# Optimization experiments

Hardware: AMD Instinct MI355X
Metric: run time of the kernel (lower is better)

The kernel has to match this reference:

```python
import jax, jax.numpy as jnp
import numpy as np

TEMPERATURE = 8.0  # sqrt(d_k=64)

def setup_inputs() -> dict:
    key = jax.random.key(0)
    kq, kk, kv, km1, km2 = jax.random.split(key, 5)
    B, Lq, Lk, D = 128, 512, 512, 64
    q = jax.random.normal(kq, (B, Lq, D), dtype=jnp.float32)
    k = jax.random.normal(kk, (B, Lk, D), dtype=jnp.float32)
    v = jax.random.normal(kv, (B, Lk, D), dtype=jnp.float32)
    key_mask = jax.random.bernoulli(km1, 0.5, (B, Lq, Lk))
    query_mask = jax.random.bernoulli(km2, 0.5, (B, Lq, Lk))
    return {"q": q, "k": k, "v": v, "key_mask": key_mask, "query_mask": query_mask}

def reference(q, k, v, key_mask, query_mask):
    # attn = (q @ k^T) / temperature, pre-softmax key masking with -inf
    scores = jnp.einsum('bqd,bkd->bqk', q, k) / TEMPERATURE
    scores = jnp.where(key_mask, -jnp.inf, scores)
    attn = jax.nn.softmax(scores, axis=-1)
    # post-softmax query-row zeroing
    attn = jnp.where(query_mask, 0.0, attn)
    # dropout omitted (eval mode / deterministic reference)
    output = jnp.einsum('bqk,bkd->bqd', attn, v)
    return (output, attn)
```

## Files before the change

kernel.cpp:

```cpp
#include <hip/hip_runtime.h>
#include <hip/hip_bf16.h>

#define BATCH 128
#define LQ    512
#define LK    512
#define DH    64
#define TQ    16
#define KC    64

#define VROW  72
#define SSTR  520

typedef float    float4v __attribute__((ext_vector_type(4)));
typedef short    short8v __attribute__((ext_vector_type(8)));
typedef short    short4v __attribute__((ext_vector_type(4)));
typedef int      int4v   __attribute__((ext_vector_type(4)));
typedef _Float16 half4v  __attribute__((ext_vector_type(4)));

__device__ __forceinline__ short bf16r(float f) {
  union { float f; unsigned u; } x; x.f = f;
  unsigned r = x.u + 0x7FFFu + ((x.u >> 16) & 1u);
  return (short)(r >> 16);
}

__global__ __launch_bounds__(256, 6)
void sdpa_kernel(const float* __restrict__ Q, const float* __restrict__ K,
                 const float* __restrict__ V, const int* __restrict__ KM,
                 const int* __restrict__ QM, float* __restrict__ OUT,
                 float* __restrict__ ATT)
{
  __shared__ short kvs[KC * VROW];
  __shared__ short scs[TQ * SSTR];

  const int bid  = blockIdx.x;
  const int wg   = ((bid & 7) << 9) | (bid >> 3);
  const int b    = wg >> 5;
  const int q0   = (wg & 31) * TQ;
  const int tid  = threadIdx.x;
  const int lane = tid & 63;
  const int wave = tid >> 6;
  const int lm   = lane & 15;
  const int quad = lane >> 4;

  const int row = tid >> 4;
  const int col = tid & 15;
  const size_t gro = (size_t)(b * LQ + q0 + row) * LK;

  int4v kmv[8];
#pragma unroll
  for (int j = 0; j < 8; ++j)
    kmv[j] = __builtin_nontemporal_load((const int4v*)(KM + gro + col * 4 + j * 64));

  const float* qrow = Q + ((size_t)(b * LQ + q0 + lm)) * DH + quad * 8;
  short8v aq0, aq1;
  {
    float4v f0 = *(const float4v*)(qrow + 0);
    float4v f1 = *(const float4v*)(qrow + 4);
    float4v f2 = *(const float4v*)(qrow + 32);
    float4v f3 = *(const float4v*)(qrow + 36);
#pragma unroll
    for (int e = 0; e < 4; ++e) {
      aq0[e]     = bf16r(f0[e]);
      aq0[e + 4] = bf16r(f1[e]);
      aq1[e]     = bf16r(f2[e]);
      aq1[e + 4] = bf16r(f3[e]);
    }
  }

#pragma unroll
  for (int t = 0; t < 8; ++t) {
    const int T = wave * 8 + t;
    const float* kr = K + ((size_t)(b * LK + T * 16 + lm)) * DH + quad * 8;
    float4v f0 = *(const float4v*)(kr + 0);
    float4v f1 = *(const float4v*)(kr + 4);
    float4v f2 = *(const float4v*)(kr + 32);
    float4v f3 = *(const float4v*)(kr + 36);
    short8v b0, b1;
#pragma unroll
    for (int e = 0; e < 4; ++e) {
      b0[e]     = bf16r(f0[e]);
      b0[e + 4] = bf16r(f1[e]);
      b1[e]     = bf16r(f2[e]);
      b1[e + 4] = bf16r(f3[e]);
    }
    float4v acc = {0.f, 0.f, 0.f, 0.f};
    acc = __builtin_amdgcn_mfma_f32_16x16x32_bf16(aq0, b0, acc, 0, 0, 0);
    acc = __builtin_amdgcn_mfma_f32_16x16x32_bf16(aq1, b1, acc, 0, 0, 0);
    const int n  = T * 16 + lm;
    const int m0 = quad * 4;
#pragma unroll
    for (int j = 0; j < 4; ++j)
      *(_Float16*)&scs[(m0 + j) * SSTR + n] = (_Float16)acc[j];
  }
  __syncthreads();

  float s[32];
  float mx = -INFINITY;
#pragma unroll
  for (int j = 0; j < 8; ++j) {
    half4v h4 = *(const half4v*)&scs[row * SSTR + col * 4 + j * 64];
#pragma unroll
    for (int e = 0; e < 4; ++e) {
      float val = kmv[j][e] ? -INFINITY : (float)h4[e];
      s[j * 4 + e] = val;
      mx = fmaxf(mx, val);
    }
  }
  int4v qmv[8];
#pragma unroll
  for (int j = 0; j < 8; ++j)
    qmv[j] = __builtin_nontemporal_load((const int4v*)(QM + gro + col * 4 + j * 64));
#pragma unroll
  for (int off = 8; off; off >>= 1) mx = fmaxf(mx, __shfl_xor(mx, off, 64));
  float sum = 0.f;
#pragma unroll
  for (int j = 0; j < 32; ++j) {
    float p = __expf((s[j] - mx) * 0.125f);
    s[j] = p;
    sum += p;
  }
#pragma unroll
  for (int off = 8; off; off >>= 1) sum += __shfl_xor(sum, off, 64);
  const float inv = 1.f / sum;
  float* arow = ATT + gro;
#pragma unroll
  for (int j = 0; j < 8; ++j) {
    int kk = col * 4 + j * 64;
    float4v a4;
#pragma unroll
    for (int e = 0; e < 4; ++e)
      a4[e] = qmv[j][e] ? 0.f : s[j * 4 + e] * inv;
    __builtin_nontemporal_store(a4, (float4v*)(arow + kk));
    short4v ab;
    ab[0] = bf16r(a4[0]); ab[1] = bf16r(a4[1]);
    ab[2] = bf16r(a4[2]); ab[3] = bf16r(a4[3]);
    *(short4v*)&scs[row * SSTR + kk] = ab;
  }

  float4v oacc = {0.f, 0.f, 0.f, 0.f};
  const float* vbase = V + ((size_t)b * LK) * DH;
  float4v va[4];
  {
    const float* vp = vbase + (row * 4) * DH + col * 4;
#pragma unroll
    for (int r = 0; r < 4; ++r) va[r] = *(const float4v*)(vp + r * DH);
  }
#pragma unroll
  for (int kt = 0; kt < 8; ++kt) {
#pragma unroll
    for (int e = 0; e < 4; ++e) {
      int d  = col * 4 + e;
      int gp = row ^ (d & 15);
      short4v s4;
      s4[0] = bf16r(va[0][e]); s4[1] = bf16r(va[1][e]);
      s4[2] = bf16r(va[2][e]); s4[3] = bf16r(va[3][e]);
      *(short4v*)&kvs[d * VROW + gp * 4] = s4;
    }
    float4v vb[4];
    if (kt < 7) {
      const float* vp = vbase + ((kt + 1) * KC + row * 4) * DH + col * 4;
#pragma unroll
      for (int r = 0; r < 4; ++r) vb[r] = *(const float4v*)(vp + r * DH);
    }
    __syncthreads();
#pragma unroll
    for (int ks = 0; ks < 2; ++ks) {
      const short* ap = &scs[lm * SSTR + kt * KC + ks * 32 + quad * 8];
      short8v a8 = *(const short8v*)ap;
      int n  = wave * 16 + lm;
      int g0 = ks * 8 + quad * 2;
      short4v lo = *(const short4v*)&kvs[n * VROW + ((g0    ) ^ (n & 15)) * 4];
      short4v hi = *(const short4v*)&kvs[n * VROW + ((g0 + 1) ^ (n & 15)) * 4];
      short8v b8;
      b8[0] = lo[0]; b8[1] = lo[1]; b8[2] = lo[2]; b8[3] = lo[3];
      b8[4] = hi[0]; b8[5] = hi[1]; b8[6] = hi[2]; b8[7] = hi[3];
      oacc = __builtin_amdgcn_mfma_f32_16x16x32_bf16(a8, b8, oacc, 0, 0, 0);
    }
    __syncthreads();
#pragma unroll
    for (int r = 0; r < 4; ++r) va[r] = vb[r];
  }
  {
    int m0 = quad * 4;
    float* obase = OUT + ((size_t)(b * LQ + q0 + m0)) * DH + wave * 16 + lm;
    obase[0 * DH] = oacc[0];
    obase[1 * DH] = oacc[1];
    obase[2 * DH] = oacc[2];
    obase[3 * DH] = oacc[3];
  }
}

extern "C" void kernel_launch(void* const* d_in, const int* in_sizes, int n_in,
                              void* d_out, int out_size, void* d_ws, size_t ws_size,
                              hipStream_t stream) {
  const float* q  = (const float*)d_in[0];
  const float* k  = (const float*)d_in[1];
  const float* v  = (const float*)d_in[2];
  const int*   km = (const int*)d_in[3];
  const int*   qm = (const int*)d_in[4];
  float* out  = (float*)d_out;
  float* attn = out + (size_t)BATCH * LQ * DH;
  dim3 grid(BATCH * (LQ / TQ));
  dim3 block(256);
  hipLaunchKernelGGL(sdpa_kernel, grid, block, 0, stream,
                     q, k, v, km, qm, out, attn);
}
```

Measured before the change: 404.2 us.

## Prefetch K tiles, bit-pack masks, split reductions, and relax launch bounds

Several changes are bundled. K tiles are now software-prefetched one step ahead during the QK^T loop, and the query-mask load is issued before the barrier instead of after the max pass. Both masks are packed into 32-bit bitfields to free registers, and the max and sum reductions use four independent accumulators to shorten dependency chains. The V prefetch is moved ahead of the LDS transpose-store, 1/sum is computed with the hardware reciprocal, and the launch-bounds occupancy hint drops from 6 to 4 blocks per CU, which trades occupancy for more registers per thread.

```diff
diff --git a/kernel.cpp b/kernel.cpp
--- a/kernel.cpp
+++ b/kernel.cpp
@@ -23,7 +23,7 @@
   return (short)(r >> 16);
 }
 
-__global__ __launch_bounds__(256, 6)
+__global__ __launch_bounds__(256, 4)
 void sdpa_kernel(const float* __restrict__ Q, const float* __restrict__ K,
                  const float* __restrict__ V, const int* __restrict__ KM,
                  const int* __restrict__ QM, float* __restrict__ OUT,
@@ -46,10 +46,10 @@
   const int col = tid & 15;
   const size_t gro = (size_t)(b * LQ + q0 + row) * LK;
 
-  int4v kmv[8];
-#pragma unroll
-  for (int j = 0; j < 8; ++j)
-    kmv[j] = __builtin_nontemporal_load((const int4v*)(KM + gro + col * 4 + j * 64));
+  int4v km8[8];
+#pragma unroll
+  for (int j = 0; j < 8; ++j)
+    km8[j] = __builtin_nontemporal_load((const int4v*)(KM + gro + col * 4 + j * 64));
 
   const float* qrow = Q + ((size_t)(b * LQ + q0 + lm)) * DH + quad * 8;
   short8v aq0, aq1;
@@ -67,61 +67,99 @@
     }
   }
 
+  unsigned kb = 0;
+#pragma unroll
+  for (int j = 0; j < 8; ++j)
+#pragma unroll
+    for (int e = 0; e < 4; ++e)
+      kb |= (unsigned)(km8[j][e] != 0) << (j * 4 + e);
+
+  const float* kbp = K + ((size_t)(b * LK + lm)) * DH + quad * 8;
+  float4v kf0, kf1, kf2, kf3;
+  {
+    const float* kr = kbp + (size_t)(wave * 8) * 16 * DH;
+    kf0 = *(const float4v*)(kr + 0);
+    kf1 = *(const float4v*)(kr + 4);
+    kf2 = *(const float4v*)(kr + 32);
+    kf3 = *(const float4v*)(kr + 36);
+  }
 #pragma unroll
   for (int t = 0; t < 8; ++t) {
-    const int T = wave * 8 + t;
-    const float* kr = K + ((size_t)(b * LK + T * 16 + lm)) * DH + quad * 8;
-    float4v f0 = *(const float4v*)(kr + 0);
-    float4v f1 = *(const float4v*)(kr + 4);
-    float4v f2 = *(const float4v*)(kr + 32);
-    float4v f3 = *(const float4v*)(kr + 36);
+    float4v kn0, kn1, kn2, kn3;
+    if (t < 7) {
+      const float* kr = kbp + (size_t)(wave * 8 + t + 1) * 16 * DH;
+      kn0 = *(const float4v*)(kr + 0);
+      kn1 = *(const float4v*)(kr + 4);
+      kn2 = *(const float4v*)(kr + 32);
+      kn3 = *(const float4v*)(kr + 36);
+    }
     short8v b0, b1;
 #pragma unroll
     for (int e = 0; e < 4; ++e) {
-      b0[e]     = bf16r(f0[e]);
-      b0[e + 4] = bf16r(f1[e]);
-      b1[e]     = bf16r(f2[e]);
-      b1[e + 4] = bf16r(f3[e]);
+      b0[e]     = bf16r(kf0[e]);
+      b0[e + 4] = bf16r(kf1[e]);
+      b1[e]     = bf16r(kf2[e]);
+      b1[e + 4] = bf16r(kf3[e]);
     }
     float4v acc = {0.f, 0.f, 0.f, 0.f};
     acc = __builtin_amdgcn_mfma_f32_16x16x32_bf16(aq0, b0, acc, 0, 0, 0);
     acc = __builtin_amdgcn_mfma_f32_16x16x32_bf16(aq1, b1, acc, 0, 0, 0);
-    const int n  = T * 16 + lm;
+    const int n  = (wave * 8 + t) * 16 + lm;
     const int m0 = quad * 4;
 #pragma unroll
     for (int j = 0; j < 4; ++j)
       *(_Float16*)&scs[(m0 + j) * SSTR + n] = (_Float16)acc[j];
-  }
+    if (t < 7) { kf0 = kn0; kf1 = kn1; kf2 = kn2; kf3 = kn3; }
+  }
+
+  int4v qm8[8];
+#pragma unroll
+  for (int j = 0; j < 8; ++j)
+    qm8[j] = __builtin_nontemporal_load((const int4v*)(QM + gro + col * 4 + j * 64));
+
   __syncthreads();
 
   float s[32];
-  float mx = -INFINITY;
+  float mx0 = -INFINITY, mx1 = -INFINITY, mx2 = -INFINITY, mx3 = -INFINITY;
 #pragma unroll
   for (int j = 0; j < 8; ++j) {
     half4v h4 = *(const half4v*)&scs[row * SSTR + col * 4 + j * 64];
 #pragma unroll
     for (int e = 0; e < 4; ++e) {
-      float val = kmv[j][e] ? -INFINITY : (float)h4[e];
+      float val = ((kb >> (j * 4 + e)) & 1u) ? -INFINITY : (float)h4[e];
       s[j * 4 + e] = val;
-      mx = fmaxf(mx, val);
-    }
-  }
-  int4v qmv[8];
-#pragma unroll
-  for (int j = 0; j < 8; ++j)
-    qmv[j] = __builtin_nontemporal_load((const int4v*)(QM + gro + col * 4 + j * 64));
+      if (e == 0) mx0 = fmaxf(mx0, val);
+      else if (e == 1) mx1 = fmaxf(mx1, val);
+      else if (e == 2) mx2 = fmaxf(mx2, val);
+      else mx3 = fmaxf(mx3, val);
+    }
+  }
+  float mx = fmaxf(fmaxf(mx0, mx1), fmaxf(mx2, mx3));
 #pragma unroll
   for (int off = 8; off; off >>= 1) mx = fmaxf(mx, __shfl_xor(mx, off, 64));
-  float sum = 0.f;
-#pragma unroll
-  for (int j = 0; j < 32; ++j) {
-    float p = __expf((s[j] - mx) * 0.125f);
-    s[j] = p;
-    sum += p;
-  }
+
+  unsigned qb = 0;
+#pragma unroll
+  for (int j = 0; j < 8; ++j)
+#pragma unroll
+    for (int e = 0; e < 4; ++e)
+      qb |= (unsigned)(qm8[j][e] != 0) << (j * 4 + e);
+
+  float s0 = 0.f, s1 = 0.f, s2 = 0.f, s3 = 0.f;
+#pragma unroll
+  for (int j = 0; j < 8; ++j) {
+    float p0 = __expf((s[j * 4 + 0] - mx) * 0.125f);
+    float p1 = __expf((s[j * 4 + 1] - mx) * 0.125f);
+    float p2 = __expf((s[j * 4 + 2] - mx) * 0.125f);
+    float p3 = __expf((s[j * 4 + 3] - mx) * 0.125f);
+    s[j * 4 + 0] = p0; s[j * 4 + 1] = p1;
+    s[j * 4 + 2] = p2; s[j * 4 + 3] = p3;
+    s0 += p0; s1 += p1; s2 += p2; s3 += p3;
+  }
+  float sum = (s0 + s1) + (s2 + s3);
 #pragma unroll
   for (int off = 8; off; off >>= 1) sum += __shfl_xor(sum, off, 64);
-  const float inv = 1.f / sum;
+  const float inv = __builtin_amdgcn_rcpf(sum);
   float* arow = ATT + gro;
 #pragma unroll
   for (int j = 0; j < 8; ++j) {
@@ -129,7 +167,7 @@
     float4v a4;
 #pragma unroll
     for (int e = 0; e < 4; ++e)
-      a4[e] = qmv[j][e] ? 0.f : s[j * 4 + e] * inv;
+      a4[e] = ((qb >> (j * 4 + e)) & 1u) ? 0.f : s[j * 4 + e] * inv;
     __builtin_nontemporal_store(a4, (float4v*)(arow + kk));
     short4v ab;
     ab[0] = bf16r(a4[0]); ab[1] = bf16r(a4[1]);
@@ -147,6 +185,12 @@
   }
 #pragma unroll
   for (int kt = 0; kt < 8; ++kt) {
+    float4v vb[4];
+    if (kt < 7) {
+      const float* vp = vbase + ((kt + 1) * KC + row * 4) * DH + col * 4;
+#pragma unroll
+      for (int r = 0; r < 4; ++r) vb[r] = *(const float4v*)(vp + r * DH);
+    }
 #pragma unroll
     for (int e = 0; e < 4; ++e) {
       int d  = col * 4 + e;
@@ -155,12 +199,6 @@
       s4[0] = bf16r(va[0][e]); s4[1] = bf16r(va[1][e]);
       s4[2] = bf16r(va[2][e]); s4[3] = bf16r(va[3][e]);
       *(short4v*)&kvs[d * VROW + gp * 4] = s4;
-    }
-    float4v vb[4];
-    if (kt < 7) {
-      const float* vp = vbase + ((kt + 1) * KC + row * 4) * DH + col * 4;
-#pragma unroll
-      for (int r = 0; r < 4; ++r) vb[r] = *(const float4v*)(vp + r * DH);
     }
     __syncthreads();
 #pragma unroll
```

After: 418.1 us. +3.4%, slower.
